# Performance work log

Hardware: AMD Instinct MI355X
Metric: run time of the kernel (lower is better)

## Reference

```python
import jax, jax.numpy as jnp
import numpy as np

D_IN, D_MODEL, DEPTH = 8, 1024, 12
D_INNER, D_STATE, D_CONV, DT_RANK = 2048, 16, 4, 64
B = 512


def setup_inputs() -> dict:
    key = jax.random.key(0)
    ks = jax.random.split(key, 12)
    f = lambda k, shp, s=0.02: jax.random.normal(k, shp, jnp.float32) * s
    inp = dict(
        x_t=jax.random.normal(ks[0], (B, D_IN), jnp.float32),
        conv_states=jax.random.normal(ks[1], (DEPTH, B, D_INNER, D_CONV), jnp.float32),
        ssm_states=jax.random.normal(ks[2], (DEPTH, B, D_INNER, D_STATE), jnp.float32),
        W_in=f(ks[3], (D_MODEL, D_IN), 0.1),
        b_in=jnp.zeros((D_MODEL,), jnp.float32),
        in_proj_w=f(ks[4], (DEPTH, 2 * D_INNER, D_MODEL)),
        conv_w=f(ks[5], (DEPTH, D_INNER, D_CONV), 0.2),
        conv_b=jnp.zeros((DEPTH, D_INNER), jnp.float32),
        x_proj_w=f(ks[6], (DEPTH, DT_RANK + 2 * D_STATE, D_INNER)),
        dt_proj_w=f(ks[7], (DEPTH, D_INNER, DT_RANK), 0.1),
        dt_proj_b=f(ks[8], (DEPTH, D_INNER), 0.5),
        # A initialized as in mamba_ssm: A = 1..d_state repeated over d_inner, A_log = log(A)
        A_log=jnp.log(jnp.tile(jnp.arange(1, D_STATE + 1, dtype=jnp.float32), (DEPTH, D_INNER, 1))),
        D_param=jnp.ones((DEPTH, D_INNER), jnp.float32),
        out_proj_w=f(ks[9], (DEPTH, D_MODEL, D_INNER)),
        ln_w=jnp.ones((D_MODEL,), jnp.float32),
        ln_b=jnp.zeros((D_MODEL,), jnp.float32),
    )
    return inp


def reference(x_t, conv_states, ssm_states, W_in, b_in, in_proj_w, conv_w, conv_b,
              x_proj_w, dt_proj_w, dt_proj_b, A_log, D_param, out_proj_w, ln_w, ln_b):
    # Backbone input projection: (B, d_in) -> (B, d_model)
    h = x_t @ W_in.T + b_in

    def layer(h, p):
        ipw, cw, cb, xpw, dtw, dtb, alog, dpar, opw, cst, sst = p
        xz = h @ ipw.T                                  # (B, 2*d_inner)
        x, z = jnp.split(xz, 2, axis=-1)                # (B, d_inner) each
        # depthwise causal conv state update (roll left, append x)
        cst = jnp.concatenate([cst[:, :, 1:], x[:, :, None]], axis=-1)  # (B, d_inner, d_conv)
        x = jax.nn.silu(jnp.sum(cst * cw[None], axis=-1) + cb)
        # input-dependent SSM params
        xdb = x @ xpw.T                                 # (B, dt_rank + 2*d_state)
        dt = xdb[:, :DT_RANK]
        Bm = xdb[:, DT_RANK:DT_RANK + D_STATE]
        Cm = xdb[:, DT_RANK + D_STATE:]
        dt = jax.nn.softplus(dt @ dtw.T + dtb)          # (B, d_inner)
        A = -jnp.exp(alog)                              # (d_inner, d_state)
        dA = jnp.exp(dt[:, :, None] * A[None])          # (B, d_inner, d_state)
        sst = sst * dA + (dt * x)[:, :, None] * Bm[:, None, :]
        y = jnp.einsum('bdn,bn->bd', sst, Cm) + dpar * x
        y = y * jax.nn.silu(z)
        return y @ opw.T, None                          # (B, d_model)

    h, _ = jax.lax.scan(
        layer, h,
        (in_proj_w, conv_w, conv_b, x_proj_w, dt_proj_w, dt_proj_b,
         A_log, D_param, out_proj_w, conv_states, ssm_states))

    # LayerNorm
    mu = jnp.mean(h, axis=-1, keepdims=True)
    var = jnp.var(h, axis=-1, keepdims=True)
    return (h - mu) / jnp.sqrt(var + 1e-5) * ln_w + ln_b
```

## Files before the change

kernel.cpp:

```cpp
#include <hip/hip_runtime.h>

#define D_IN 8
#define D_MODEL 1024
#define DEPTH 12
#define D_INNER 2048
#define D_STATE 16
#define D_CONV 4
#define DT_RANK 64
#define BATCH 512

typedef unsigned short ushort_t;
typedef unsigned int uint_t;
typedef __attribute__((ext_vector_type(8))) short short8;
typedef __attribute__((ext_vector_type(16))) float f32x16;

#if defined(__has_builtin)
#if __has_builtin(__builtin_amdgcn_global_load_lds)
#define USE_GLL 1
#endif
#endif

__device__ __forceinline__ float sigmoidf_(float x) { return 1.f / (1.f + expf(-x)); }
__device__ __forceinline__ float siluf_(float x) { return x * sigmoidf_(x); }
__device__ __forceinline__ float softplusf_(float x) { return fmaxf(x, 0.f) + log1pf(expf(-fabsf(x))); }

__device__ __forceinline__ float waveRedSum(float v) {
#pragma unroll
  for (int off = 32; off; off >>= 1) v += __shfl_xor(v, off);
  return v;
}

__device__ __forceinline__ ushort_t f2bf(float x) {
  uint_t u = __float_as_uint(x);
  u += 0x7fffu + ((u >> 16) & 1u);
  return (ushort_t)(u >> 16);
}
__device__ __forceinline__ float bf2f(ushort_t h) { return __uint_as_float((uint_t)h << 16); }
__device__ __forceinline__ void split3(float x, ushort_t& s0, ushort_t& s1, ushort_t& s2) {
  s0 = f2bf(x); float r = x - bf2f(s0);
  s1 = f2bf(r); r -= bf2f(s1);
  s2 = f2bf(r);
}
__device__ __forceinline__ uint4 pack8(const ushort_t* u) {
  uint4 v;
  v.x = (uint_t)u[0] | ((uint_t)u[1] << 16);
  v.y = (uint_t)u[2] | ((uint_t)u[3] << 16);
  v.z = (uint_t)u[4] | ((uint_t)u[5] << 16);
  v.w = (uint_t)u[6] | ((uint_t)u[7] << 16);
  return v;
}

__device__ __forceinline__ int slotx(int row, int slot) { return slot ^ ((row >> 1) & 3); }

__device__ __forceinline__ void stage16(const ushort_t* gbase, ushort_t* lbase, int lane) {
#ifdef USE_GLL
  __builtin_amdgcn_global_load_lds(
      (const __attribute__((address_space(1))) unsigned int*)(gbase + lane * 8),
      (__attribute__((address_space(3))) unsigned int*)lbase, 16, 0, 0);
#else
  *(uint4*)(lbase + lane * 8) = *(const uint4*)(gbase + lane * 8);
#endif
}

__global__ __launch_bounds__(256) void k_presplit(const float* __restrict__ W,
    ushort_t* __restrict__ Bt, int K, int items) {
  const int KB = K >> 5;
  for (int i = blockIdx.x * 256 + threadIdx.x; i < items; i += gridDim.x * 256) {
    const int kpr = K >> 3;
    const int n = i / kpr, k0 = (i - n * kpr) * 8;
    const float* g = W + (size_t)n * K + k0;
    float fv[8];
    *(float4*)&fv[0] = *(const float4*)(g + 0);
    *(float4*)&fv[4] = *(const float4*)(g + 4);
    ushort_t u0[8], u1[8], u2[8];
#pragma unroll
    for (int j = 0; j < 8; ++j) split3(fv[j], u0[j], u1[j], u2[j]);
    const int nb = n >> 7, r = n & 127, kb = k0 >> 5;
    const int so = slotx(r, (k0 >> 3) & 3) * 8;
    const size_t dst = ((size_t)(nb * KB + kb) * 3) * 4096 + r * 32 + so;
    *(uint4*)&Bt[dst]        = pack8(u0);
    *(uint4*)&Bt[dst + 4096] = pack8(u1);
    *(uint4*)&Bt[dst + 8192] = pack8(u2);
  }
}

__global__ __launch_bounds__(256) void k_negA(const float* __restrict__ alog,
    float* __restrict__ negA, int items) {
  int i = blockIdx.x * 256 + threadIdx.x;
  if (i < items) negA[i] = -expf(alog[i]);
}

__global__ __launch_bounds__(256) void k_input_proj(const float* __restrict__ xt,
    const float* __restrict__ Win, const float* __restrict__ bin,
    ushort_t* __restrict__ h_t) {
  int idx = blockIdx.x * 256 + threadIdx.x;
  int b = idx >> 10, m = idx & 1023;
  float acc = bin[m];
  const float* xr = xt + b * D_IN;
  const float* wr = Win + m * D_IN;
#pragma unroll
  for (int k = 0; k < D_IN; ++k) acc += xr[k] * wr[k];
  ushort_t s0, s1, s2; split3(acc, s0, s1, s2);
  const int mb = b >> 6, r = b & 63, kb = m >> 5;
  const int so = slotx(r, (m >> 3) & 3) * 8;
  const size_t base = ((size_t)(mb * 32 + kb) * 3) * 2048 + r * 32 + so + (m & 7);
  h_t[base] = s0; h_t[base + 2048] = s1; h_t[base + 4096] = s2;
}

template <int MBLK, int NBLK, int KSPLIT, int KB>
__global__ __launch_bounds__(256, 4) void k_gemm6(
    const ushort_t* __restrict__ At, const ushort_t* __restrict__ Bt,
    float* __restrict__ P, int N) {
  __shared__ __align__(16) ushort_t lds[18432];
  const int t = threadIdx.x, lane = t & 63, w = t >> 6;
  const int wm = w >> 1;
  const int ks = w & 1;

  constexpr int GRID = MBLK * NBLK * KSPLIT;
  constexpr int STEPS = KB / KSPLIT;
  const int id = blockIdx.x;
  const int swz = (id & 7) * (GRID >> 3) + (id >> 3);
  const int kb = swz / (MBLK * NBLK);
  const int r2 = swz % (MBLK * NBLK);
  const int mb = r2 % MBLK, nb = r2 / MBLK;

  f32x16 acc[2][2];
#pragma unroll
  for (int i = 0; i < 2; ++i)
#pragma unroll
    for (int j = 0; j < 2; ++j)
#pragma unroll
      for (int r = 0; r < 16; ++r) acc[i][j][r] = 0.f;

  for (int step = 0; step < STEPS; ++step) {
    const int kt = kb * STEPS + step;
    const ushort_t* gA = At + ((size_t)(mb * KB + kt)) * 6144;
    const ushort_t* gB = Bt + ((size_t)(nb * KB + kt)) * 12288;
    __syncthreads();
#pragma unroll
    for (int i = 0; i < 9; ++i) {
      const int c = w + i * 4;
      const ushort_t* src = (c < 12) ? (gA + c * 512) : (gB + (c - 12) * 512);
      stage16(src, &lds[c * 512], lane);
    }
    __syncthreads();

    const int kslot = ks * 2 + (lane >> 5);
    short8 af[2][3], bf[2][3];
#pragma unroll
    for (int mf = 0; mf < 2; ++mf) {
      const int r = mf * 32 + (lane & 31);
      const int so = slotx(r, kslot) * 8;
#pragma unroll
      for (int s = 0; s < 3; ++s)
        af[mf][s] = *(const short8*)&lds[s * 2048 + r * 32 + so];
    }
#pragma unroll
    for (int nf = 0; nf < 2; ++nf) {
      const int r = wm * 64 + nf * 32 + (lane & 31);
      const int so = slotx(r, kslot) * 8;
#pragma unroll
      for (int s = 0; s < 3; ++s)
        bf[nf][s] = *(const short8*)&lds[6144 + s * 4096 + r * 32 + so];
    }
#pragma unroll
    for (int mf = 0; mf < 2; ++mf)
#pragma unroll
      for (int nf = 0; nf < 2; ++nf) {
        acc[mf][nf] = __builtin_amdgcn_mfma_f32_32x32x16_bf16(af[mf][0], bf[nf][0], acc[mf][nf], 0, 0, 0);
        acc[mf][nf] = __builtin_amdgcn_mfma_f32_32x32x16_bf16(af[mf][0], bf[nf][1], acc[mf][nf], 0, 0, 0);
        acc[mf][nf] = __builtin_amdgcn_mfma_f32_32x32x16_bf16(af[mf][1], bf[nf][0], acc[mf][nf], 0, 0, 0);
        acc[mf][nf] = __builtin_amdgcn_mfma_f32_32x32x16_bf16(af[mf][1], bf[nf][1], acc[mf][nf], 0, 0, 0);
        acc[mf][nf] = __builtin_amdgcn_mfma_f32_32x32x16_bf16(af[mf][2], bf[nf][0], acc[mf][nf], 0, 0, 0);
        acc[mf][nf] = __builtin_amdgcn_mfma_f32_32x32x16_bf16(af[mf][0], bf[nf][2], acc[mf][nf], 0, 0, 0);
      }
  }

  __syncthreads();
  float* red = (float*)lds;
  const int rbase = (wm * 64 + lane) * 68;
  if (ks == 1) {
#pragma unroll
    for (int j = 0; j < 16; ++j) {
      const int mf = j >> 3, nf = (j >> 2) & 1, r0 = (j & 3) * 4;
      float4 v;
      v.x = acc[mf][nf][r0 + 0]; v.y = acc[mf][nf][r0 + 1];
      v.z = acc[mf][nf][r0 + 2]; v.w = acc[mf][nf][r0 + 3];
      *(float4*)&red[rbase + j * 4] = v;
    }
  }
  __syncthreads();
  if (ks == 0) {
#pragma unroll
    for (int j = 0; j < 16; ++j) {
      const int mf = j >> 3, nf = (j >> 2) & 1, r0 = (j & 3) * 4;
      float4 v = *(const float4*)&red[rbase + j * 4];
      acc[mf][nf][r0 + 0] += v.x; acc[mf][nf][r0 + 1] += v.y;
      acc[mf][nf][r0 + 2] += v.z; acc[mf][nf][r0 + 3] += v.w;
    }
    float* Pk = P + (size_t)kb * 512 * N;
    const int n0 = nb * 128, m0 = mb * 64;
#pragma unroll
    for (int mf = 0; mf < 2; ++mf) {
      const int n = n0 + wm * 64 + (lane & 31);
#pragma unroll
      for (int nf = 0; nf < 2; ++nf)
#pragma unroll
        for (int r = 0; r < 16; ++r) {
          const int m = m0 + mf * 32 + (r & 3) + 8 * (r >> 2) + 4 * (lane >> 5);
          Pk[(size_t)m * N + n + nf * 32] = acc[mf][nf][r];
        }
    }
  }
}

__global__ __launch_bounds__(256) void k_fused(
    const float* __restrict__ Pin,
    const float* __restrict__ cst, const float* __restrict__ sst,
    const float* __restrict__ cw, const float* __restrict__ cb,
    const float* __restrict__ xpw, const float* __restrict__ dtw, const float* __restrict__ dtb,
    const float* __restrict__ negA, const float* __restrict__ dpar,
    ushort_t* __restrict__ y_t) {
  __shared__ float sxc[D_INNER];
  __shared__ float sxdb[96];
  const int t = threadIdx.x;
  const int b = blockIdx.x;
  const size_t S = 2097152;

  for (int d = t; d < D_INNER; d += 256) {
    float4 c = *(const float4*)&cst[((size_t)b * D_INNER + d) * 4];
    float4 w = *(const float4*)&cw[d * 4];
    const size_t xi = (size_t)b * 4096 + d;
    float xv = Pin[xi] + Pin[xi + S] + Pin[xi + 2 * S] + Pin[xi + 3 * S];
    float a = c.y * w.x + c.z * w.y + c.w * w.z + xv * w.w + cb[d];
    sxc[d] = siluf_(a);
  }
  __syncthreads();

  const int wave = t >> 6, lane = t & 63;
  const int lane4 = lane * 4;
  for (int r0 = wave * 24; r0 < wave * 24 + 24; r0 += 2) {
    const float* w0 = &xpw[(size_t)r0 * D_INNER];
    const float* w1 = w0 + D_INNER;
    float a0 = 0.f, a1 = 0.f, c0 = 0.f, c1 = 0.f;
#pragma unroll
    for (int it = 0; it < 8; ++it) {
      const int k = it * 256 + lane4;
      float4 x  = *(const float4*)&sxc[k];
      float4 wa = *(const float4*)&w0[k];
      float4 wb = *(const float4*)&w1[k];
      a0 += wa.x * x.x + wa.y * x.y;  a1 += wa.z * x.z + wa.w * x.w;
      c0 += wb.x * x.x + wb.y * x.y;  c1 += wb.z * x.z + wb.w * x.w;
    }
    float ra = waveRedSum(a0 + a1);
    float rb = waveRedSum(c0 + c1);
    if (lane == 0) { sxdb[r0] = ra; sxdb[r0 + 1] = rb; }
  }
  __syncthreads();

  for (int d = t; d < D_INNER; d += 256) {
    float dtr = dtb[d];
#pragma unroll
    for (int j4 = 0; j4 < DT_RANK / 4; ++j4) {
      float4 wv = *(const float4*)&dtw[(size_t)d * DT_RANK + j4 * 4];
      dtr += sxdb[j4 * 4] * wv.x + sxdb[j4 * 4 + 1] * wv.y +
             sxdb[j4 * 4 + 2] * wv.z + sxdb[j4 * 4 + 3] * wv.w;
    }
    float dtv = softplusf_(dtr);
    float xcv = sxc[d];
    float dx = dtv * xcv;
    const float4* srow4 = (const float4*)&sst[((size_t)b * D_INNER + d) * D_STATE];
    const float4* na4 = (const float4*)&negA[(size_t)d * D_STATE];
    float acc = 0.f;
#pragma unroll
    for (int q = 0; q < 4; ++q) {
      float4 sv = srow4[q];
      float4 na = na4[q];
      float4 Bn = *(const float4*)&sxdb[DT_RANK + q * 4];
      float4 Cn = *(const float4*)&sxdb[DT_RANK + D_STATE + q * 4];
      acc += (sv.x * expf(dtv * na.x) + dx * Bn.x) * Cn.x;
      acc += (sv.y * expf(dtv * na.y) + dx * Bn.y) * Cn.y;
      acc += (sv.z * expf(dtv * na.z) + dx * Bn.z) * Cn.z;
      acc += (sv.w * expf(dtv * na.w) + dx * Bn.w) * Cn.w;
    }
    float yv = acc + dpar[d] * xcv;
    const size_t zi = (size_t)b * 4096 + D_INNER + d;
    float zv = Pin[zi] + Pin[zi + S] + Pin[zi + 2 * S] + Pin[zi + 3 * S];
    yv *= siluf_(zv);
    ushort_t s0, s1, s2; split3(yv, s0, s1, s2);
    const int mb = b >> 6, r = b & 63, kb = d >> 5;
    const int so = slotx(r, (d >> 3) & 3) * 8;
    const size_t base = ((size_t)(mb * 64 + kb) * 3) * 2048 + r * 32 + so + (d & 7);
    y_t[base] = s0; y_t[base + 2048] = s1; y_t[base + 4096] = s2;
  }
}

__global__ __launch_bounds__(256) void k_reduce_out(const float* __restrict__ P,
    float* __restrict__ h, ushort_t* __restrict__ h_t) {
  const int i = blockIdx.x * 256 + threadIdx.x;
  float4 a = ((const float4*)P)[i];
#pragma unroll
  for (int p = 1; p < 16; ++p) {
    float4 b = ((const float4*)P)[(size_t)p * 131072 + i];
    a.x += b.x; a.y += b.y; a.z += b.z; a.w += b.w;
  }
  ((float4*)h)[i] = a;
  float fv[4] = {a.x, a.y, a.z, a.w};
  ushort_t u0[4], u1[4], u2[4];
#pragma unroll
  for (int j = 0; j < 4; ++j) split3(fv[j], u0[j], u1[j], u2[j]);
  const int flat = i * 4;
  const int b = flat >> 10, k = flat & 1023;
  const int mb = b >> 6, r = b & 63, kb = k >> 5;
  const int so = slotx(r, (k >> 3) & 3) * 8;
  const size_t base = ((size_t)(mb * 32 + kb) * 3) * 2048 + r * 32 + so + (k & 7);
  *(uint2*)&h_t[base]        = make_uint2((uint_t)u0[0] | ((uint_t)u0[1] << 16), (uint_t)u0[2] | ((uint_t)u0[3] << 16));
  *(uint2*)&h_t[base + 2048] = make_uint2((uint_t)u1[0] | ((uint_t)u1[1] << 16), (uint_t)u1[2] | ((uint_t)u1[3] << 16));
  *(uint2*)&h_t[base + 4096] = make_uint2((uint_t)u2[0] | ((uint_t)u2[1] << 16), (uint_t)u2[2] | ((uint_t)u2[3] << 16));
}

__global__ __launch_bounds__(256) void k_layernorm(const float* __restrict__ h,
    const float* __restrict__ lnw, const float* __restrict__ lnb, float* __restrict__ out) {
  __shared__ float red[4];
  const int b = blockIdx.x, t = threadIdx.x;
  const float* row = h + (size_t)b * D_MODEL;
  float4 x = *(const float4*)&row[t * 4];
  float s = x.x + x.y + x.z + x.w;
  s = waveRedSum(s);
  const int wave = t >> 6, lane = t & 63;
  if (lane == 0) red[wave] = s;
  __syncthreads();
  float mu = (red[0] + red[1] + red[2] + red[3]) * (1.f / 1024.f);
  float d0 = x.x - mu, d1 = x.y - mu, d2 = x.z - mu, d3 = x.w - mu;
  float q = d0 * d0 + d1 * d1 + d2 * d2 + d3 * d3;
  q = waveRedSum(q);
  __syncthreads();
  if (lane == 0) red[wave] = q;
  __syncthreads();
  float var = (red[0] + red[1] + red[2] + red[3]) * (1.f / 1024.f);
  float inv = 1.f / sqrtf(var + 1e-5f);
  float4 wv = *(const float4*)&lnw[t * 4];
  float4 bv = *(const float4*)&lnb[t * 4];
  float4 o;
  o.x = d0 * inv * wv.x + bv.x;
  o.y = d1 * inv * wv.y + bv.y;
  o.z = d2 * inv * wv.z + bv.z;
  o.w = d3 * inv * wv.w + bv.w;
  *(float4*)&out[(size_t)b * D_MODEL + t * 4] = o;
}

extern "C" void kernel_launch(void* const* d_in, const int* in_sizes, int n_in,
                              void* d_out, int out_size, void* d_ws, size_t ws_size,
                              hipStream_t stream) {
  const float* x_t  = (const float*)d_in[0];
  const float* cst  = (const float*)d_in[1];
  const float* sst  = (const float*)d_in[2];
  const float* Win  = (const float*)d_in[3];
  const float* bin  = (const float*)d_in[4];
  const float* ipw  = (const float*)d_in[5];
  const float* cw   = (const float*)d_in[6];
  const float* cb   = (const float*)d_in[7];
  const float* xpw  = (const float*)d_in[8];
  const float* dtw  = (const float*)d_in[9];
  const float* dtb  = (const float*)d_in[10];
  const float* alog = (const float*)d_in[11];
  const float* dpar = (const float*)d_in[12];
  const float* opw  = (const float*)d_in[13];
  const float* lnw  = (const float*)d_in[14];
  const float* lnb  = (const float*)d_in[15];

  float* ws   = (float*)d_ws;
  float* h    = ws;
  float* Pin  = h + 524288;
  float* Pout = Pin + 8388608;
  float* negA = Pout + 8388608;
  ushort_t* u = (ushort_t*)(negA + 393216);
  ushort_t* h_t = u;
  ushort_t* y_t = h_t + 1572864;
  ushort_t* iw_t = y_t + 3145728;
  ushort_t* ow_t = iw_t + 150994944;

  k_presplit<<<2048, 256, 0, stream>>>(ipw, iw_t, 1024, 12 * 524288);
  k_presplit<<<2048, 256, 0, stream>>>(opw, ow_t, 2048, 12 * 262144);
  k_negA<<<1536, 256, 0, stream>>>(alog, negA, 12 * D_INNER * D_STATE);
  k_input_proj<<<2048, 256, 0, stream>>>(x_t, Win, bin, h_t);

  for (int l = 0; l < DEPTH; ++l) {
    const ushort_t* iw = iw_t + (size_t)l * 12582912;
    const ushort_t* ow = ow_t + (size_t)l * 6291456;
    k_gemm6<8, 32, 4, 32><<<1024, 256, 0, stream>>>(h_t, iw, Pin, 4096);
    k_fused<<<512, 256, 0, stream>>>(
        Pin,
        cst + (size_t)l * BATCH * D_INNER * D_CONV,
        sst + (size_t)l * BATCH * D_INNER * D_STATE,
        cw + (size_t)l * D_INNER * D_CONV, cb + (size_t)l * D_INNER,
        xpw + (size_t)l * 96 * D_INNER,
        dtw + (size_t)l * D_INNER * DT_RANK, dtb + (size_t)l * D_INNER,
        negA + (size_t)l * D_INNER * D_STATE, dpar + (size_t)l * D_INNER,
        y_t);
    k_gemm6<8, 8, 16, 64><<<1024, 256, 0, stream>>>(y_t, ow, Pout, 1024);
    k_reduce_out<<<512, 256, 0, stream>>>(Pout, h, h_t);
  }

  k_layernorm<<<512, 256, 0, stream>>>(h, lnw, lnb, (float*)d_out);
}
```

Measured before the change: 1.859 ms.

## Fuse split-K reduction into GEMM via last-block atomic counter

Each split-K GEMM block now bumps a per-tile atomic counter after writing its partial sums. The last block to finish a tile sums all K-slices and writes the final output, which is the xz buffer for the in-projection and h plus the split h_t for the out-projection. This removes the separate reduce_out kernel and the 4-way partial-sum reads in k_fused. The cost is threadfences, atomics, a per-layer memset of the counters, and a serialized tail reduction done by the last block of each tile.

```diff
diff --git a/kernel.cpp b/kernel.cpp
--- a/kernel.cpp
+++ b/kernel.cpp
@@ -107,11 +107,13 @@
   h_t[base] = s0; h_t[base + 2048] = s1; h_t[base + 4096] = s2;
 }
 
-template <int MBLK, int NBLK, int KSPLIT, int KB>
+template <int MBLK, int NBLK, int KSPLIT, int KB, int MODE>
 __global__ __launch_bounds__(256, 4) void k_gemm6(
     const ushort_t* __restrict__ At, const ushort_t* __restrict__ Bt,
-    float* __restrict__ P, int N) {
+    float* __restrict__ P, float* __restrict__ out, ushort_t* __restrict__ out_t,
+    uint_t* cnt, int N) {
   __shared__ __align__(16) ushort_t lds[18432];
+  __shared__ uint_t lastFlag;
   const int t = threadIdx.x, lane = t & 63, w = t >> 6;
   const int wm = w >> 1;
   const int ks = w & 1;
@@ -212,10 +214,51 @@
         }
     }
   }
+
+  __threadfence();
+  __syncthreads();
+  if (t == 0) {
+    uint_t ret = __hip_atomic_fetch_add(&cnt[mb * NBLK + nb], 1u,
+                                        __ATOMIC_ACQ_REL, __HIP_MEMORY_SCOPE_AGENT);
+    lastFlag = (ret == KSPLIT - 1) ? 1u : 0u;
+  }
+  __syncthreads();
+  if (lastFlag) {
+    const int m0 = mb * 64, n0 = nb * 128;
+    const size_t SLICE = (size_t)512 * N;
+#pragma unroll
+    for (int i = 0; i < 8; ++i) {
+      const int idx = i * 256 + t;
+      const int m = idx >> 5, c4 = idx & 31;
+      const size_t off = (size_t)(m0 + m) * N + n0 + c4 * 4;
+      float4 a = *(const float4*)&P[off];
+#pragma unroll
+      for (int p = 1; p < KSPLIT; ++p) {
+        float4 bv = *(const float4*)&P[p * SLICE + off];
+        a.x += bv.x; a.y += bv.y; a.z += bv.z; a.w += bv.w;
+      }
+      if constexpr (MODE == 0) {
+        *(float4*)&out[off] = a;
+      } else {
+        *(float4*)&out[off] = a;
+        float fv[4] = {a.x, a.y, a.z, a.w};
+        ushort_t u0[4], u1[4], u2[4];
+#pragma unroll
+        for (int j = 0; j < 4; ++j) split3(fv[j], u0[j], u1[j], u2[j]);
+        const int r = m;
+        const int k0 = n0 + c4 * 4;
+        const size_t base = ((size_t)(mb * 32 + (k0 >> 5)) * 3) * 2048
+                            + r * 32 + slotx(r, (k0 >> 3) & 3) * 8 + (k0 & 7);
+        *(uint2*)&out_t[base]        = make_uint2((uint_t)u0[0] | ((uint_t)u0[1] << 16), (uint_t)u0[2] | ((uint_t)u0[3] << 16));
+        *(uint2*)&out_t[base + 2048] = make_uint2((uint_t)u1[0] | ((uint_t)u1[1] << 16), (uint_t)u1[2] | ((uint_t)u1[3] << 16));
+        *(uint2*)&out_t[base + 4096] = make_uint2((uint_t)u2[0] | ((uint_t)u2[1] << 16), (uint_t)u2[2] | ((uint_t)u2[3] << 16));
+      }
+    }
+  }
 }
 
 __global__ __launch_bounds__(256) void k_fused(
-    const float* __restrict__ Pin,
+    const float* __restrict__ xz,
     const float* __restrict__ cst, const float* __restrict__ sst,
     const float* __restrict__ cw, const float* __restrict__ cb,
     const float* __restrict__ xpw, const float* __restrict__ dtw, const float* __restrict__ dtb,
@@ -225,13 +268,11 @@
   __shared__ float sxdb[96];
   const int t = threadIdx.x;
   const int b = blockIdx.x;
-  const size_t S = 2097152;
 
   for (int d = t; d < D_INNER; d += 256) {
     float4 c = *(const float4*)&cst[((size_t)b * D_INNER + d) * 4];
     float4 w = *(const float4*)&cw[d * 4];
-    const size_t xi = (size_t)b * 4096 + d;
-    float xv = Pin[xi] + Pin[xi + S] + Pin[xi + 2 * S] + Pin[xi + 3 * S];
+    float xv = xz[(size_t)b * 4096 + d];
     float a = c.y * w.x + c.z * w.y + c.w * w.z + xv * w.w + cb[d];
     sxc[d] = siluf_(a);
   }
@@ -284,8 +325,7 @@
       acc += (sv.w * expf(dtv * na.w) + dx * Bn.w) * Cn.w;
     }
     float yv = acc + dpar[d] * xcv;
-    const size_t zi = (size_t)b * 4096 + D_INNER + d;
-    float zv = Pin[zi] + Pin[zi + S] + Pin[zi + 2 * S] + Pin[zi + 3 * S];
+    float zv = xz[(size_t)b * 4096 + D_INNER + d];
     yv *= siluf_(zv);
     ushort_t s0, s1, s2; split3(yv, s0, s1, s2);
     const int mb = b >> 6, r = b & 63, kb = d >> 5;
@@ -293,30 +333,6 @@
     const size_t base = ((size_t)(mb * 64 + kb) * 3) * 2048 + r * 32 + so + (d & 7);
     y_t[base] = s0; y_t[base + 2048] = s1; y_t[base + 4096] = s2;
   }
-}
-
-__global__ __launch_bounds__(256) void k_reduce_out(const float* __restrict__ P,
-    float* __restrict__ h, ushort_t* __restrict__ h_t) {
-  const int i = blockIdx.x * 256 + threadIdx.x;
-  float4 a = ((const float4*)P)[i];
-#pragma unroll
-  for (int p = 1; p < 16; ++p) {
-    float4 b = ((const float4*)P)[(size_t)p * 131072 + i];
-    a.x += b.x; a.y += b.y; a.z += b.z; a.w += b.w;
-  }
-  ((float4*)h)[i] = a;
-  float fv[4] = {a.x, a.y, a.z, a.w};
-  ushort_t u0[4], u1[4], u2[4];
-#pragma unroll
-  for (int j = 0; j < 4; ++j) split3(fv[j], u0[j], u1[j], u2[j]);
-  const int flat = i * 4;
-  const int b = flat >> 10, k = flat & 1023;
-  const int mb = b >> 6, r = b & 63, kb = k >> 5;
-  const int so = slotx(r, (k >> 3) & 3) * 8;
-  const size_t base = ((size_t)(mb * 32 + kb) * 3) * 2048 + r * 32 + so + (k & 7);
-  *(uint2*)&h_t[base]        = make_uint2((uint_t)u0[0] | ((uint_t)u0[1] << 16), (uint_t)u0[2] | ((uint_t)u0[3] << 16));
-  *(uint2*)&h_t[base + 2048] = make_uint2((uint_t)u1[0] | ((uint_t)u1[1] << 16), (uint_t)u1[2] | ((uint_t)u1[3] << 16));
-  *(uint2*)&h_t[base + 4096] = make_uint2((uint_t)u2[0] | ((uint_t)u2[1] << 16), (uint_t)u2[2] | ((uint_t)u2[3] << 16));
 }
 
 __global__ __launch_bounds__(256) void k_layernorm(const float* __restrict__ h,
@@ -371,14 +387,18 @@
 
   float* ws   = (float*)d_ws;
   float* h    = ws;
-  float* Pin  = h + 524288;
+  float* xz   = h + 524288;
+  float* Pin  = xz + 2097152;
   float* Pout = Pin + 8388608;
   float* negA = Pout + 8388608;
-  ushort_t* u = (ushort_t*)(negA + 393216);
+  uint_t* cnt = (uint_t*)(negA + 393216);
+  ushort_t* u = (ushort_t*)(cnt + 512);
   ushort_t* h_t = u;
   ushort_t* y_t = h_t + 1572864;
   ushort_t* iw_t = y_t + 3145728;
   ushort_t* ow_t = iw_t + 150994944;
+  uint_t* cnt_in  = cnt;
+  uint_t* cnt_out = cnt + 256;
 
   k_presplit<<<2048, 256, 0, stream>>>(ipw, iw_t, 1024, 12 * 524288);
   k_presplit<<<2048, 256, 0, stream>>>(opw, ow_t, 2048, 12 * 262144);
@@ -388,9 +408,11 @@
   for (int l = 0; l < DEPTH; ++l) {
     const ushort_t* iw = iw_t + (size_t)l * 12582912;
     const ushort_t* ow = ow_t + (size_t)l * 6291456;
-    k_gemm6<8, 32, 4, 32><<<1024, 256, 0, stream>>>(h_t, iw, Pin, 4096);
+    hipMemsetAsync(cnt, 0, 1280, stream);
+    k_gemm6<8, 32, 4, 32, 0><<<1024, 256, 0, stream>>>(
+        h_t, iw, Pin, xz, nullptr, cnt_in, 4096);
     k_fused<<<512, 256, 0, stream>>>(
-        Pin,
+        xz,
         cst + (size_t)l * BATCH * D_INNER * D_CONV,
         sst + (size_t)l * BATCH * D_INNER * D_STATE,
         cw + (size_t)l * D_INNER * D_CONV, cb + (size_t)l * D_INNER,
@@ -398,8 +420,8 @@
         dtw + (size_t)l * D_INNER * DT_RANK, dtb + (size_t)l * D_INNER,
         negA + (size_t)l * D_INNER * D_STATE, dpar + (size_t)l * D_INNER,
         y_t);
-    k_gemm6<8, 8, 16, 64><<<1024, 256, 0, stream>>>(y_t, ow, Pout, 1024);
-    k_reduce_out<<<512, 256, 0, stream>>>(Pout, h, h_t);
+    k_gemm6<8, 8, 16, 64, 1><<<1024, 256, 0, stream>>>(
+        y_t, ow, Pout, h, h_t, cnt_out, 1024);
   }
 
   k_layernorm<<<512, 256, 0, stream>>>(h, lnw, lnb, (float*)d_out);
```

Result: slower. 5.831 ms (+213.6%).
